# Optimization experiments

Measured on AMD Instinct MI355X. Metric: run time of the kernel, lower is better.

Reference implementation:

```python
import jax, jax.numpy as jnp
import numpy as np

WS = 7
NH = 8
ROPE_FREQ = 100.0


def _rope2d(tokens, positions, freq=ROPE_FREQ):
    # CroCo-style RoPE2D. tokens: [Bw, nh, T, hd]; positions: [Bw, T, 2] int (y, x).
    d = tokens.shape[-1] // 2
    inv = 1.0 / (freq ** (jnp.arange(0, d, 2, dtype=jnp.float32) / d))  # [d/2]

    def rope1d(t, pos):
        ang = pos[..., None].astype(jnp.float32) * inv            # [Bw, T, d/2]
        ang = jnp.concatenate([ang, ang], -1)[:, None]            # [Bw, 1, T, d]
        cos, sin = jnp.cos(ang), jnp.sin(ang)
        x1, x2 = jnp.split(t, 2, axis=-1)
        return t * cos + jnp.concatenate([-x2, x1], -1) * sin

    return jnp.concatenate(
        [rope1d(tokens[..., :d], positions[..., 0]),
         rope1d(tokens[..., d:], positions[..., 1])], -1)


def _qkv(t, w, b, nh):
    Bt, Tt, C = t.shape
    hd = C // nh
    y = (t @ w.T + b).reshape(Bt, Tt, 3, nh, hd).transpose(2, 0, 3, 1, 4)
    return y[0], y[1], y[2]


def _attn(q, k, v, scale):
    a = jax.nn.softmax(jnp.einsum('bhqd,bhkd->bhqk', q, k) * scale, axis=-1)
    return jnp.einsum('bhqk,bhkd->bhqd', a, v)


def setup_inputs() -> dict:
    key = jax.random.key(0)
    ks = jax.random.split(key, 6)
    B, H, W, C, A = 8, 112, 112, 256, 16
    N = H * W + A
    return {
        'x': jax.random.normal(ks[0], (B, N, C), jnp.float32),
        'pos2d': jax.random.randint(ks[1], (B, N, 2), 0, 112, jnp.int32),
        'rope_mask': jnp.ones((B, N), jnp.bool_),
        'qkv_w': jax.random.normal(ks[2], (3 * C, C), jnp.float32) * 0.02,
        'qkv_b': jax.random.normal(ks[3], (3 * C,), jnp.float32) * 0.02,
        'proj_w': jax.random.normal(ks[4], (C, C), jnp.float32) * 0.02,
        'proj_b': jax.random.normal(ks[5], (C,), jnp.float32) * 0.02,
        'grid_h': 112,
        'grid_w': 112,
        'num_added_tokens': 16,
    }


def reference(x, pos2d, rope_mask, qkv_w, qkv_b, proj_w, proj_b, grid_h, grid_w, num_added_tokens):
    B, N, C = x.shape
    H, W, ws, nh = grid_h, grid_w, WS, NH
    hd = C // nh
    scale = hd ** (-0.5)
    HW = H * W
    x_sp, x_add = x[:, :HW], x[:, HW:]
    pos_sp = pos2d[:, :HW]
    mask_sp = rope_mask[:, :HW]

    nWh, nWw = H // ws, W // ws  # H, W divisible by ws (no padding)

    def part(t):  # [B, HW, F] -> [B*nW, ws*ws, F]
        F_ = t.shape[-1]
        t = t.reshape(B, nWh, ws, nWw, ws, F_).transpose(0, 1, 3, 2, 4, 5)
        return t.reshape(B * nWh * nWw, ws * ws, F_)

    xw = part(x_sp)                                   # [Bw, 49, C]
    pw = part(pos_sp)                                 # [Bw, 49, 2]
    mw = part(mask_sp[..., None].astype(jnp.float32))[..., 0] > 0.5  # [Bw, 49]

    q, k, v = _qkv(xw, qkv_w, qkv_b, nh)              # each [Bw, nh, 49, hd]
    qr, kr = _rope2d(q, pw), _rope2d(k, pw)
    m = mw[:, None, :, None]
    q = jnp.where(m, qr, q)
    k = jnp.where(m, kr, k)

    Bw, T = xw.shape[0], ws * ws
    ow = _attn(q, k, v, scale).transpose(0, 2, 1, 3).reshape(Bw, T, C)
    ow = ow @ proj_w.T + proj_b

    # window reverse
    x2 = ow.reshape(B, nWh, nWw, ws, ws, C).transpose(0, 1, 3, 2, 4, 5).reshape(B, HW, C)

    if num_added_tokens > 0:
        qa, ka, va = _qkv(x_add, qkv_w, qkv_b, nh)    # [B, nh, A, hd]
        qs, ks, vs = _qkv(x2, qkv_w, qkv_b, nh)       # [B, nh, HW, hd]
        o_add = _attn(qa, ks, vs, scale).transpose(0, 2, 1, 3).reshape(B, num_added_tokens, C)
        o_add = o_add @ proj_w.T + proj_b
        upd = _attn(qs, ka, va, scale).transpose(0, 2, 1, 3).reshape(B, HW, C)
        upd = upd @ proj_w.T + proj_b
        x2 = x2 + upd * 0.5
        return jnp.concatenate([x2, o_add], axis=1)
    return x2
```

## Files before the change

kernel.cpp:

```cpp
#include <hip/hip_runtime.h>
#include <hip/hip_bf16.h>


typedef __hip_bfloat16 bf16;
typedef __attribute__((ext_vector_type(8))) short short8v;
typedef __attribute__((ext_vector_type(8))) unsigned short ushort8v;
typedef __attribute__((ext_vector_type(4))) float f32x4;

#define HW_TOK 12544
#define NTOK   12560
#define ATT_SCALE 0.17677669529663687f

__device__ __forceinline__ int lwin_to_tok(int wt) {
    int w = wt / 49, t = wt - w * 49;
    int wr = w >> 4, wc = w & 15;
    int r = t / 7, c = t - r * 7;
    return (wr * 7 + r) * 112 + (wc * 7 + c);
}

__device__ __forceinline__ float b2f(unsigned short u) {
    unsigned int w = ((unsigned int)u) << 16;
    return *reinterpret_cast<float*>(&w);
}
__device__ __forceinline__ unsigned short f2b(float v) {
    bf16 h = __float2bfloat16(v);
    return *reinterpret_cast<unsigned short*>(&h);
}

template<bool F32>
__device__ __forceinline__ float ldv(const void* p, size_t i) {
    if constexpr (F32) return reinterpret_cast<const float*>(p)[i];
    else return b2f(reinterpret_cast<const unsigned short*>(p)[i]);
}
template<bool F32>
__device__ __forceinline__ float4 ldv4(const void* p, size_t i) {
    if constexpr (F32) {
        return *reinterpret_cast<const float4*>(reinterpret_cast<const float*>(p) + i);
    } else {
        ushort4 u = *reinterpret_cast<const ushort4*>(
            reinterpret_cast<const unsigned short*>(p) + i);
        return float4{b2f(u.x), b2f(u.y), b2f(u.z), b2f(u.w)};
    }
}
template<bool F32>
__device__ __forceinline__ void stv(void* p, size_t i, float v) {
    if constexpr (F32) reinterpret_cast<float*>(p)[i] = v;
    else reinterpret_cast<unsigned short*>(p)[i] = f2b(v);
}
template<bool F32>
__device__ __forceinline__ void stv4(void* p, size_t i, float4 v) {
    if constexpr (F32) {
        *reinterpret_cast<float4*>(reinterpret_cast<float*>(p) + i) = v;
    } else {
        ushort4 u{f2b(v.x), f2b(v.y), f2b(v.z), f2b(v.w)};
        *reinterpret_cast<ushort4*>(reinterpret_cast<unsigned short*>(p) + i) = u;
    }
}

__global__ void probe_dtype(const unsigned short* x, int n_elem, int* flag) {
    int tid = threadIdx.x;
    int stride = (n_elem / 2048) & ~1;
    if (stride < 2) stride = 2;
    int insane = 0;
    for (int s = 0; s < 8; ++s) {
        long idx = (long)(tid * 8 + s) * stride;
        if (idx >= n_elem) idx = idx % n_elem & ~1L;
        unsigned short u = x[idx];
        unsigned e = (u >> 7) & 0xFF;
        if (e == 0xFF || e >= 141 || (e >= 1 && e <= 112)) insane++;
    }
    __shared__ int tot;
    if (tid == 0) tot = 0;
    __syncthreads();
    atomicAdd(&tot, insane);
    __syncthreads();
    if (tid == 0) flag[0] = (tot > 512) ? 1 : 0;
}

__global__ __launch_bounds__(256) void k_tab(float2* tab) {
    int idx = blockIdx.x * 256 + threadIdx.x;
    if (idx >= 112 * 8) return;
    int p = idx >> 3, i = idx & 7;
    float inv = exp2f((float)i * -0.8304820237218407f);
    float ang = (float)p * inv;
    float sn, cs; sincosf(ang, &sn, &cs);
    tab[idx] = float2{cs, sn};
}

__device__ __forceinline__ f32x4 mfma_bb(short8v a, short8v b, f32x4 c) {
    return __builtin_amdgcn_mfma_f32_16x16x32_bf16(a, b, c, 0, 0, 0);
}
__device__ __forceinline__ f32x4 mfma3(short8v aH, short8v aL,
                                       short8v bH, short8v bL, f32x4 c) {
    c = mfma_bb(aH, bH, c);
    c = mfma_bb(aH, bL, c);
    c = mfma_bb(aL, bH, c);
    return c;
}

__device__ __forceinline__ void cvt8(float4 f0, float4 f1,
                                     ushort8v& hi, ushort8v& lo) {
    float ff[8] = {f0.x, f0.y, f0.z, f0.w, f1.x, f1.y, f1.z, f1.w};
    #pragma unroll
    for (int i = 0; i < 8; ++i) {
        unsigned short h = f2b(ff[i]);
        hi[i] = h;
        lo[i] = f2b(ff[i] - b2f(h));
    }
}

struct __align__(16) GemmLDS {
    unsigned short AsH[128 * 32];
    unsigned short AsL[128 * 32];
    unsigned short BsH[128 * 32];
    unsigned short BsL[128 * 32];
};

__device__ __forceinline__ int lds_idx32(int row, int ks) {
    int byte = (ks * 2) ^ ((row & 3) << 4);
    return row * 32 + (byte >> 1);
}

template<bool F32>
__device__ __forceinline__ void gemm128(
    GemmLDS& L, const void* A, size_t arow, const void* B, size_t brow_,
    f32x4 (&acc)[4][4], int tid)
{
    const int lane = tid & 63, wave = tid >> 6;
    const int wr = (wave >> 1) * 64, wc = (wave & 1) * 64;
    const int fr = lane & 15, fkb = (lane >> 4) * 8;
    const int tr = tid >> 1, tk = (tid & 1) * 16;
    const size_t ab = arow + tk, bb = brow_ + tk;

    float4 pa0, pa1, pa2, pa3, pb0, pb1, pb2, pb3;
    #define LOADCH(K0) do { \
        pa0 = ldv4<F32>(A, ab + (K0));      pa1 = ldv4<F32>(A, ab + (K0) + 4);  \
        pa2 = ldv4<F32>(A, ab + (K0) + 8);  pa3 = ldv4<F32>(A, ab + (K0) + 12); \
        pb0 = ldv4<F32>(B, bb + (K0));      pb1 = ldv4<F32>(B, bb + (K0) + 4);  \
        pb2 = ldv4<F32>(B, bb + (K0) + 8);  pb3 = ldv4<F32>(B, bb + (K0) + 12); \
    } while (0)

    LOADCH(0);
    for (int t = 0; t < 8; ++t) {
        __builtin_amdgcn_s_barrier();
        __builtin_amdgcn_sched_barrier(0);
        ushort8v h, l;
        cvt8(pa0, pa1, h, l);
        *reinterpret_cast<ushort8v*>(&L.AsH[lds_idx32(tr, tk)]) = h;
        *reinterpret_cast<ushort8v*>(&L.AsL[lds_idx32(tr, tk)]) = l;
        cvt8(pa2, pa3, h, l);
        *reinterpret_cast<ushort8v*>(&L.AsH[lds_idx32(tr, tk + 8)]) = h;
        *reinterpret_cast<ushort8v*>(&L.AsL[lds_idx32(tr, tk + 8)]) = l;
        cvt8(pb0, pb1, h, l);
        *reinterpret_cast<ushort8v*>(&L.BsH[lds_idx32(tr, tk)]) = h;
        *reinterpret_cast<ushort8v*>(&L.BsL[lds_idx32(tr, tk)]) = l;
        cvt8(pb2, pb3, h, l);
        *reinterpret_cast<ushort8v*>(&L.BsH[lds_idx32(tr, tk + 8)]) = h;
        *reinterpret_cast<ushort8v*>(&L.BsL[lds_idx32(tr, tk + 8)]) = l;
        if (t < 7) LOADCH((t + 1) * 32);
        asm volatile("s_waitcnt lgkmcnt(0)" ::: "memory");
        __builtin_amdgcn_s_barrier();
        __builtin_amdgcn_sched_barrier(0);
        short8v bH[4], bL[4], aH, aL;
        #pragma unroll
        for (int j = 0; j < 4; ++j) {
            bH[j] = *reinterpret_cast<const short8v*>(&L.BsH[lds_idx32(wc + j * 16 + fr, fkb)]);
            bL[j] = *reinterpret_cast<const short8v*>(&L.BsL[lds_idx32(wc + j * 16 + fr, fkb)]);
        }
        #pragma unroll
        for (int i = 0; i < 4; ++i) {
            aH = *reinterpret_cast<const short8v*>(&L.AsH[lds_idx32(wr + i * 16 + fr, fkb)]);
            aL = *reinterpret_cast<const short8v*>(&L.AsL[lds_idx32(wr + i * 16 + fr, fkb)]);
            #pragma unroll
            for (int j = 0; j < 4; ++j)
                acc[i][j] = mfma3(aH, aL, bH[j], bL[j], acc[i][j]);
        }
    }
    #undef LOADCH
}

__device__ __forceinline__ void epi_coords(int tid, int& rb, int& cb) {
    int lane = tid & 63, wave = tid >> 6;
    rb = (wave >> 1) * 64 + ((lane >> 4) << 2);
    cb = (wave & 1) * 64 + (lane & 15);
}

template<bool F32>
__device__ void k1_body(GemmLDS& L, const void* x, const void* w,
                        const void* bias, void* qkvb, size_t qstride, int b0) {
    int tid = threadIdx.x;
    int n0 = blockIdx.x * 128, m0 = blockIdx.y * 128;
    int z = blockIdx.z, b = b0 + z;
    int tr = tid >> 1;
    size_t arow = (size_t)(b * NTOK + lwin_to_tok(m0 + tr)) * 256;
    size_t brow = (size_t)(n0 + tr) * 256;
    f32x4 acc[4][4] = {};
    gemm128<F32>(L, x, arow, w, brow, acc, tid);
    int rb, cb; epi_coords(tid, rb, cb);
    size_t zb = (size_t)z * qstride;
    #pragma unroll
    for (int j = 0; j < 4; ++j) {
        int n = n0 + cb + j * 16;
        float bi = ldv<F32>(bias, n);
        #pragma unroll
        for (int i = 0; i < 4; ++i)
            #pragma unroll
            for (int r = 0; r < 4; ++r)
                stv<F32>(qkvb, zb + (size_t)(m0 + rb + i * 16 + r) * 768 + n,
                         acc[i][j][r] + bi);
    }
}
__global__ __launch_bounds__(256, 3) void k1_qkv_win(
    const void* x, const void* w, const void* bia, void* qkvb,
    unsigned long long qstride, int b0, const int* flag) {
    __shared__ GemmLDS L;
    if (flag[0]) k1_body<true >(L, x, w, bia, qkvb, qstride, b0);
    else         k1_body<false>(L, x, w, bia, qkvb, qstride, b0);
}

struct K3LDS {
    union {
        struct { unsigned short QH[2048], QL[2048], KH[2048], KL[2048]; } qk;
        struct { unsigned short PH[4096], PL[4096]; } p;
    } u;
    unsigned short VtH[2048], VtL[2048];
};
__device__ __forceinline__ int qk_us(int row, int d) {
    int q16 = (d >> 3) ^ (row & 3);
    return row * 32 + q16 * 8 + (d & 7);
}
__device__ __forceinline__ int p_us(int row, int kk) {
    int q16 = (kk >> 3) ^ (row & 7);
    return row * 64 + q16 * 8 + (kk & 7);
}
__device__ __forceinline__ int vt_us(int d, int kk) {
    int q16 = (kk >> 3) ^ (d & 7);
    return d * 64 + q16 * 8 + (kk & 7);
}

template<bool F32>
__device__ void k3_body(K3LDS& Ld, const void* qkvb, size_t qstride,
                        const int* pos2d, const float2* tab,
                        void* owin, size_t ostride, int b0) {
    int wb = blockIdx.x, h = blockIdx.y, tid = threadIdx.x;
    int z = blockIdx.z, b = b0 + z;
    size_t zq = (size_t)z * qstride, zo = (size_t)z * ostride;
    int lane = tid & 63, w = tid >> 6;
    int l15 = lane & 15, g = lane >> 4;
    int tokbase = ((wb >> 4) * 7) * 112 + (wb & 15) * 7;

    {
        ushort8v z8 = {0, 0, 0, 0, 0, 0, 0, 0};
        ushort8v* vz = reinterpret_cast<ushort8v*>(Ld.VtH);
        for (int e = tid; e < 512; e += 256) vz[e] = z8;
    }
    __syncthreads();

    for (int e0 = tid; e0 < 1280; e0 += 256) {
        int act = (e0 < 1176) ? 1 : 0;
        unsigned ec = act ? (unsigned)e0 : 0u;
        unsigned t = ec / 24u;
        unsigned q = ec - t * 24u;
        int seg = q >> 3, dq = q & 7;
        size_t base = zq + (size_t)(wb * 49 + t) * 768 + seg * 256 + h * 32 + dq * 4;
        float4 f4 = act ? ldv4<F32>(qkvb, base) : float4{0.f, 0.f, 0.f, 0.f};
        if (seg < 2) {
            float4 pf;
            pf.x = __shfl_xor(f4.x, 2); pf.y = __shfl_xor(f4.y, 2);
            pf.z = __shfl_xor(f4.z, 2); pf.w = __shfl_xor(f4.w, 2);
            int half = dq >> 2;
            unsigned r7 = t / 7u, c7 = t - r7 * 7u;
            int ntok = tokbase + (int)r7 * 112 + (int)c7;
            int pos = act ? pos2d[((size_t)b * NTOK + ntok) * 2 + half] : 0;
            const float2* tb = tab + pos * 8 + (dq & 1) * 4;
            float2 s0 = tb[0], s1 = tb[1], s2 = tb[2], s3 = tb[3];
            float sgn = (dq & 2) ? 1.f : -1.f;
            float4 ro;
            ro.x = f4.x * s0.x + sgn * pf.x * s0.y;
            ro.y = f4.y * s1.x + sgn * pf.y * s1.y;
            ro.z = f4.z * s2.x + sgn * pf.z * s2.y;
            ro.w = f4.w * s3.x + sgn * pf.w * s3.y;
            ushort4 hv, lv;
            hv.x = f2b(ro.x); lv.x = f2b(ro.x - b2f(hv.x));
            hv.y = f2b(ro.y); lv.y = f2b(ro.y - b2f(hv.y));
            hv.z = f2b(ro.z); lv.z = f2b(ro.z - b2f(hv.z));
            hv.w = f2b(ro.w); lv.w = f2b(ro.w - b2f(hv.w));
            if (act) {
                unsigned short* H  = seg ? Ld.u.qk.KH : Ld.u.qk.QH;
                unsigned short* Lo = seg ? Ld.u.qk.KL : Ld.u.qk.QL;
                int ua = qk_us(t, dq * 4);
                *reinterpret_cast<ushort4*>(&H[ua])  = hv;
                *reinterpret_cast<ushort4*>(&Lo[ua]) = lv;
            }
        } else if (act) {
            float vv[4] = {f4.x, f4.y, f4.z, f4.w};
            #pragma unroll
            for (int c = 0; c < 4; ++c) {
                int d = dq * 4 + c;
                unsigned short hh = f2b(vv[c]);
                Ld.VtH[vt_us(d, t)] = hh;
                Ld.VtL[vt_us(d, t)] = f2b(vv[c] - b2f(hh));
            }
        }
    }
    __syncthreads();

    f32x4 s[4];
    {
        short8v qH = *reinterpret_cast<const short8v*>(&Ld.u.qk.QH[qk_us(w * 16 + l15, g * 8)]);
        short8v qL = *reinterpret_cast<const short8v*>(&Ld.u.qk.QL[qk_us(w * 16 + l15, g * 8)]);
        #pragma unroll
        for (int j = 0; j < 4; ++j) {
            short8v kH = *reinterpret_cast<const short8v*>(&Ld.u.qk.KH[qk_us(j * 16 + l15, g * 8)]);
            short8v kL = *reinterpret_cast<const short8v*>(&Ld.u.qk.KL[qk_us(j * 16 + l15, g * 8)]);
            f32x4 zz = {0.f, 0.f, 0.f, 0.f};
            s[j] = mfma3(qH, qL, kH, kL, zz);
        }
    }
    #pragma unroll
    for (int j = 0; j < 4; ++j) {
        bool ok = (j * 16 + l15) < 49;
        #pragma unroll
        for (int r = 0; r < 4; ++r)
            s[j][r] = ok ? s[j][r] * ATT_SCALE : -1e30f;
    }
    float rr[4];
    #pragma unroll
    for (int r = 0; r < 4; ++r) {
        float m = fmaxf(fmaxf(s[0][r], s[1][r]), fmaxf(s[2][r], s[3][r]));
        m = fmaxf(m, __shfl_xor(m, 1));
        m = fmaxf(m, __shfl_xor(m, 2));
        m = fmaxf(m, __shfl_xor(m, 4));
        m = fmaxf(m, __shfl_xor(m, 8));
        float sum = 0.f;
        #pragma unroll
        for (int j = 0; j < 4; ++j) {
            float p = __expf(s[j][r] - m);
            s[j][r] = p;
            sum += p;
        }
        sum += __shfl_xor(sum, 1);
        sum += __shfl_xor(sum, 2);
        sum += __shfl_xor(sum, 4);
        sum += __shfl_xor(sum, 8);
        rr[r] = 1.0f / sum;
    }
    __syncthreads();
    #pragma unroll
    for (int j = 0; j < 4; ++j) {
        int col = j * 16 + l15;
        #pragma unroll
        for (int r = 0; r < 4; ++r) {
            int row = w * 16 + 4 * g + r;
            float p = s[j][r] * rr[r];
            unsigned short hh = f2b(p);
            Ld.u.p.PH[p_us(row, col)] = hh;
            Ld.u.p.PL[p_us(row, col)] = f2b(p - b2f(hh));
        }
    }
    __syncthreads();
    f32x4 o[2] = {};
    #pragma unroll
    for (int ks = 0; ks < 2; ++ks) {
        int k0 = ks * 32 + g * 8;
        short8v aH = *reinterpret_cast<const short8v*>(&Ld.u.p.PH[p_us(w * 16 + l15, k0)]);
        short8v aL = *reinterpret_cast<const short8v*>(&Ld.u.p.PL[p_us(w * 16 + l15, k0)]);
        #pragma unroll
        for (int nb = 0; nb < 2; ++nb) {
            short8v bH = *reinterpret_cast<const short8v*>(&Ld.VtH[vt_us(nb * 16 + l15, k0)]);
            short8v bL = *reinterpret_cast<const short8v*>(&Ld.VtL[vt_us(nb * 16 + l15, k0)]);
            o[nb] = mfma3(aH, aL, bH, bL, o[nb]);
        }
    }
    #pragma unroll
    for (int nb = 0; nb < 2; ++nb) {
        int d = nb * 16 + l15;
        #pragma unroll
        for (int r = 0; r < 4; ++r) {
            int row = w * 16 + 4 * g + r;
            if (row < 49)
                stv<F32>(owin, zo + (size_t)(wb * 49 + row) * 256 + h * 32 + d,
                         o[nb][r]);
        }
    }
}
__global__ __launch_bounds__(256, 4) void k3_winattn(
    const void* qkvb, unsigned long long qstride, const int* pos2d,
    const float2* tab, void* owin, unsigned long long ostride, int b0,
    const int* flag) {
    __shared__ K3LDS Ld;
    if (flag[0]) k3_body<true >(Ld, qkvb, qstride, pos2d, tab, owin, ostride, b0);
    else         k3_body<false>(Ld, qkvb, qstride, pos2d, tab, owin, ostride, b0);
}

template<bool F32>
__device__ void k4_body(GemmLDS& L, const void* owin, size_t ostride,
                        const void* w, const void* bias, void* out, int b0) {
    int tid = threadIdx.x;
    int n0 = blockIdx.x * 128, m0 = blockIdx.y * 128;
    int z = blockIdx.z, b = b0 + z;
    int tr = tid >> 1;
    size_t arow = (size_t)z * ostride + (size_t)(m0 + tr) * 256;
    size_t brow = (size_t)(n0 + tr) * 256;
    f32x4 acc[4][4] = {};
    gemm128<F32>(L, owin, arow, w, brow, acc, tid);
    int rb, cb; epi_coords(tid, rb, cb);
    size_t rdst[4][4];
    #pragma unroll
    for (int i = 0; i < 4; ++i)
        #pragma unroll
        for (int r = 0; r < 4; ++r)
            rdst[i][r] = (size_t)(b * NTOK + lwin_to_tok(m0 + rb + i * 16 + r)) * 256;
    #pragma unroll
    for (int j = 0; j < 4; ++j) {
        int n = n0 + cb + j * 16;
        float bi = ldv<F32>(bias, n);
        #pragma unroll
        for (int i = 0; i < 4; ++i)
            #pragma unroll
            for (int r = 0; r < 4; ++r)
                stv<F32>(out, rdst[i][r] + n, acc[i][j][r] + bi);
    }
}
__global__ __launch_bounds__(256, 3) void k4_proj_win(
    const void* owin, unsigned long long ostride, const void* w,
    const void* bia, void* out, int b0, const int* flag) {
    __shared__ GemmLDS L;
    if (flag[0]) k4_body<true >(L, owin, ostride, w, bia, out, b0);
    else         k4_body<false>(L, owin, ostride, w, bia, out, b0);
}

template<bool F32>
__device__ void k5d_body(GemmLDS& L, const void* src, const void* w,
                         const void* bias, void* qkvb, size_t qstride, int b0) {
    int tid = threadIdx.x;
    int n0 = blockIdx.x * 128, m0 = blockIdx.y * 128;
    int z = blockIdx.z, b = b0 + z;
    int tr = tid >> 1;
    size_t arow = ((size_t)b * NTOK + m0 + tr) * 256;
    size_t brow = (size_t)(n0 + tr) * 256;
    f32x4 acc[4][4] = {};
    gemm128<F32>(L, src, arow, w, brow, acc, tid);
    int rb, cb; epi_coords(tid, rb, cb);
    size_t zb = (size_t)z * qstride;
    #pragma unroll
    for (int j = 0; j < 4; ++j) {
        int n = n0 + cb + j * 16;
        float bi = ldv<F32>(bias, n);
        #pragma unroll
        for (int i = 0; i < 4; ++i)
            #pragma unroll
            for (int r = 0; r < 4; ++r)
                stv<F32>(qkvb, zb + (size_t)(m0 + rb + i * 16 + r) * 768 + n,
                         acc[i][j][r] + bi);
    }
}
__global__ __launch_bounds__(256, 3) void k5_dense(
    const void* src, const void* w, const void* bia, void* qkvb,
    unsigned long long qstride, int b0, const int* flag) {
    __shared__ GemmLDS L;
    if (flag[0]) k5d_body<true >(L, src, w, bia, qkvb, qstride, b0);
    else         k5d_body<false>(L, src, w, bia, qkvb, qstride, b0);
}

template<bool F32>
__device__ void k5a_body(GemmLDS& L, const void* x, const void* w,
                         const void* bias, void* dstq, size_t aqbs, int aqroff) {
    int tid = threadIdx.x;
    int n0 = blockIdx.x * 128;
    int tr = tid >> 1;
    int bb = tr >> 4, a = tr & 15;
    size_t arow = ((size_t)bb * NTOK + HW_TOK + a) * 256;
    size_t brow = (size_t)(n0 + tr) * 256;
    f32x4 acc[4][4] = {};
    gemm128<F32>(L, x, arow, w, brow, acc, tid);
    int rb, cb; epi_coords(tid, rb, cb);
    #pragma unroll
    for (int j = 0; j < 4; ++j) {
        int n = n0 + cb + j * 16;
        float bi = ldv<F32>(bias, n);
        #pragma unroll
        for (int i = 0; i < 4; ++i)
            #pragma unroll
            for (int r = 0; r < 4; ++r) {
                int row = rb + i * 16 + r;
                int rbb = row >> 4, ra = row & 15;
                stv<F32>(dstq, (size_t)rbb * aqbs + (size_t)(aqroff + ra) * 768 + n,
                         acc[i][j][r] + bi);
            }
    }
}
__global__ __launch_bounds__(256, 3) void k5_add(
    const void* x, const void* w, const void* bia, void* dstq,
    unsigned long long aqbs, int aqroff, const int* flag) {
    __shared__ GemmLDS L;
    if (flag[0]) k5a_body<true >(L, x, w, bia, dstq, aqbs, aqroff);
    else         k5a_body<false>(L, x, w, bia, dstq, aqbs, aqroff);
}

template<bool F32>
__device__ void k6p_body(const void* addq, size_t aqbs, int aqroff,
                         const void* qkvb, size_t qstride,
                         float* part, size_t pstride, int b0) {
    int h = blockIdx.x, s = blockIdx.y, tid = threadIdx.x;
    int z = blockIdx.z, b = b0 + z;
    size_t zq = (size_t)z * qstride;
    float* pz = part + (size_t)z * pstride;
    __shared__ __align__(16) float qa[16][32];
    __shared__ __align__(16) float ks[49][36];
    __shared__ __align__(16) float vs[49][36];
    __shared__ float S[16][52];
    __shared__ float mrow[16], lrow[16], crow[16];
    int aq = tid >> 3, adg = (tid & 7) * 4;
    if (tid < 128) {
        float4 qv = ldv4<F32>(addq, (size_t)b * aqbs +
                              (size_t)(aqroff + aq) * 768 + h * 32 + adg);
        *reinterpret_cast<float4*>(&qa[aq][adg]) = qv;
    }
    if (tid < 16) { mrow[tid] = -1e30f; lrow[tid] = 0.f; }
    float4 acc{0.f, 0.f, 0.f, 0.f};
    __syncthreads();
    for (int c = 0; c < 4; ++c) {
        int row0 = s * 196 + c * 49;
        for (int e = tid; e < 49 * 8; e += 256) {
            int j = e >> 3, dg = (e & 7) * 4;
            size_t base = zq + (size_t)(row0 + j) * 768 + 256 + h * 32 + dg;
            *reinterpret_cast<float4*>(&ks[j][dg]) = ldv4<F32>(qkvb, base);
            *reinterpret_cast<float4*>(&vs[j][dg]) = ldv4<F32>(qkvb, base + 256);
        }
        __syncthreads();
        for (int e = tid; e < 784; e += 256) {
            int q = e / 49, j = e - q * 49;
            float a = 0.f;
            #pragma unroll
            for (int dg = 0; dg < 8; ++dg) {
                float4 qv = *reinterpret_cast<const float4*>(&qa[q][dg * 4]);
                float4 kv = *reinterpret_cast<const float4*>(&ks[j][dg * 4]);
                a = fmaf(qv.x, kv.x, a); a = fmaf(qv.y, kv.y, a);
                a = fmaf(qv.z, kv.z, a); a = fmaf(qv.w, kv.w, a);
            }
            S[q][j] = a * ATT_SCALE;
        }
        __syncthreads();
        if (tid < 16) {
            float m = mrow[tid], sm = m;
            for (int j = 0; j < 49; ++j) sm = fmaxf(sm, S[tid][j]);
            float corr = expf(m - sm);
            float l = lrow[tid] * corr;
            for (int j = 0; j < 49; ++j) { float p = expf(S[tid][j] - sm); S[tid][j] = p; l += p; }
            mrow[tid] = sm; lrow[tid] = l; crow[tid] = corr;
        }
        __syncthreads();
        if (tid < 128) {
            float cr = crow[aq];
            acc.x *= cr; acc.y *= cr; acc.z *= cr; acc.w *= cr;
            for (int j = 0; j < 49; ++j) {
                float p = S[aq][j];
                float4 v = *reinterpret_cast<const float4*>(&vs[j][adg]);
                acc.x = fmaf(p, v.x, acc.x); acc.y = fmaf(p, v.y, acc.y);
                acc.z = fmaf(p, v.z, acc.z); acc.w = fmaf(p, v.w, acc.w);
            }
        }
        __syncthreads();
    }
    size_t pb = (size_t)(h * 64 + s) * 544;
    if (tid < 128)
        *reinterpret_cast<float4*>(&pz[pb + tid * 4]) = acc;
    if (tid < 16) { pz[pb + 512 + tid] = mrow[tid]; pz[pb + 528 + tid] = lrow[tid]; }
}
__global__ __launch_bounds__(256) void k6_oadd_part(
    const void* addq, unsigned long long aqbs, int aqroff,
    const void* qkvb, unsigned long long qstride,
    float* part, unsigned long long pstride, int b0, const int* flag) {
    if (flag[0]) k6p_body<true >(addq, aqbs, aqroff, qkvb, qstride, part, pstride, b0);
    else         k6p_body<false>(addq, aqbs, aqroff, qkvb, qstride, part, pstride, b0);
}

template<bool F32>
__device__ void k6mb_body(const float* part, size_t pstride,
                          const void* pw, const void* pbias, void* out, int b0) {
    int r = blockIdx.x;
    int zb = r >> 4, a = r & 15;
    int b = b0 + zb;
    const float* P = part + (size_t)zb * pstride;
    int tid = threadIdx.x;
    int h = tid >> 5, d = tid & 31;
    float M = -1e30f;
    for (int s = 0; s < 64; ++s)
        M = fmaxf(M, P[(size_t)(h * 64 + s) * 544 + 512 + a]);
    float o = 0.f, Lsum = 0.f;
    for (int s = 0; s < 64; ++s) {
        size_t pbs = (size_t)(h * 64 + s) * 544;
        float wgt = expf(P[pbs + 512 + a] - M);
        o = fmaf(wgt, P[pbs + a * 32 + d], o);
        Lsum = fmaf(wgt, P[pbs + 528 + a], Lsum);
    }
    __shared__ __align__(16) float orow[256];
    orow[tid] = o / Lsum;
    __syncthreads();
    float acc = ldv<F32>(pbias, tid);
    #pragma unroll 4
    for (int kg = 0; kg < 64; ++kg) {
        float4 w4 = ldv4<F32>(pw, (size_t)tid * 256 + kg * 4);
        float4 o4 = *reinterpret_cast<const float4*>(&orow[kg * 4]);
        acc = fmaf(o4.x, w4.x, acc); acc = fmaf(o4.y, w4.y, acc);
        acc = fmaf(o4.z, w4.z, acc); acc = fmaf(o4.w, w4.w, acc);
    }
    stv<F32>(out, ((size_t)b * NTOK + HW_TOK + a) * 256 + tid, acc);
}
__global__ __launch_bounds__(256) void k6_merge_proj(
    const float* part, unsigned long long pstride, const void* pw,
    const void* pbias, void* out, int b0, const int* flag) {
    if (flag[0]) k6mb_body<true >(part, pstride, pw, pbias, out, b0);
    else         k6mb_body<false>(part, pstride, pw, pbias, out, b0);
}

template<bool F32>
__device__ void k7_body(const void* addq, size_t aqbs, int aqroff,
                        const void* qkvb, size_t qstride,
                        void* updb, size_t ostride, int b0) {
    int tid = threadIdx.x;
    int n0 = blockIdx.x * 32;
    int z = blockIdx.y, b = b0 + z;
    size_t zq = (size_t)z * qstride, zo = (size_t)z * ostride;
    __shared__ __align__(16) float ka[8][16][32];
    __shared__ __align__(16) float va[8][16][32];
    float* kaf = &ka[0][0][0];
    float* vaf = &va[0][0][0];
    for (int e = tid; e < 1024; e += 256) {
        int g = e * 4;
        int h2 = g >> 9, rem = g & 511, a = rem >> 5, d = rem & 31;
        size_t base = (size_t)b * aqbs + (size_t)(aqroff + a) * 768 + 256 + h2 * 32 + d;
        *reinterpret_cast<float4*>(&kaf[g]) = ldv4<F32>(addq, base);
        *reinterpret_cast<float4*>(&vaf[g]) = ldv4<F32>(addq, base + 256);
    }
    __syncthreads();
    int tok = tid & 31, h = tid >> 5;
    int rowl = n0 + tok;
    float q[32];
    #pragma unroll
    for (int dg = 0; dg < 8; ++dg) {
        float4 q4 = ldv4<F32>(qkvb, zq + (size_t)rowl * 768 + h * 32 + dg * 4);
        q[dg * 4 + 0] = q4.x; q[dg * 4 + 1] = q4.y;
        q[dg * 4 + 2] = q4.z; q[dg * 4 + 3] = q4.w;
    }
    float s[16];
    float mx = -1e30f;
    #pragma unroll
    for (int a = 0; a < 16; ++a) {
        float acc = 0.f;
        #pragma unroll
        for (int d = 0; d < 32; ++d) acc = fmaf(q[d], ka[h][a][d], acc);
        s[a] = acc * ATT_SCALE; mx = fmaxf(mx, s[a]);
    }
    float sum = 0.f;
    #pragma unroll
    for (int a = 0; a < 16; ++a) { s[a] = expf(s[a] - mx); sum += s[a]; }
    float r = 1.0f / sum;
    #pragma unroll
    for (int a = 0; a < 16; ++a) s[a] *= r;
    #pragma unroll
    for (int dg = 0; dg < 8; ++dg) {
        float4 o{0.f, 0.f, 0.f, 0.f};
        #pragma unroll
        for (int a = 0; a < 16; ++a) {
            float p = s[a];
            o.x = fmaf(p, va[h][a][dg * 4 + 0], o.x);
            o.y = fmaf(p, va[h][a][dg * 4 + 1], o.y);
            o.z = fmaf(p, va[h][a][dg * 4 + 2], o.z);
            o.w = fmaf(p, va[h][a][dg * 4 + 3], o.w);
        }
        stv4<F32>(updb, zo + (size_t)rowl * 256 + h * 32 + dg * 4, o);
    }
}
__global__ __launch_bounds__(256) void k7_upd(
    const void* addq, unsigned long long aqbs, int aqroff,
    const void* qkvb, unsigned long long qstride,
    void* updb, unsigned long long ostride, int b0, const int* flag) {
    if (flag[0]) k7_body<true >(addq, aqbs, aqroff, qkvb, qstride, updb, ostride, b0);
    else         k7_body<false>(addq, aqbs, aqroff, qkvb, qstride, updb, ostride, b0);
}

template<bool F32>
__device__ void k8_body(GemmLDS& L, const void* updb, size_t ostride,
                        const void* w, const void* bias, void* out, int b0) {
    int tid = threadIdx.x;
    int n0 = blockIdx.x * 128, m0 = blockIdx.y * 128;
    int z = blockIdx.z, b = b0 + z;
    int tr = tid >> 1;
    size_t arow = (size_t)z * ostride + (size_t)(m0 + tr) * 256;
    size_t brow = (size_t)(n0 + tr) * 256;
    f32x4 acc[4][4] = {};
    gemm128<F32>(L, updb, arow, w, brow, acc, tid);
    int rb, cb; epi_coords(tid, rb, cb);
    #pragma unroll
    for (int j = 0; j < 4; ++j) {
        int n = n0 + cb + j * 16;
        float bi = ldv<F32>(bias, n);
        #pragma unroll
        for (int i = 0; i < 4; ++i)
            #pragma unroll
            for (int r = 0; r < 4; ++r) {
                size_t obase = ((size_t)b * NTOK + m0 + rb + i * 16 + r) * 256 + n;
                float xv = ldv<F32>(out, obase);
                stv<F32>(out, obase, xv + 0.5f * (acc[i][j][r] + bi));
            }
    }
}
__global__ __launch_bounds__(256, 3) void k8_final(
    const void* updb, unsigned long long ostride, const void* w,
    const void* bia, void* out, int b0, const int* flag) {
    __shared__ GemmLDS L;
    if (flag[0]) k8_body<true >(L, updb, ostride, w, bia, out, b0);
    else         k8_body<false>(L, updb, ostride, w, bia, out, b0);
}

extern "C" void kernel_launch(void* const* d_in, const int* in_sizes, int n_in,
                              void* d_out, int out_size, void* d_ws, size_t ws_size,
                              hipStream_t stream) {
    const void* x      = d_in[0];
    const int*  pos2d  = (const int*)d_in[1];
    const void* qkv_w  = d_in[3];
    const void* qkv_b  = d_in[4];
    const void* proj_w = d_in[5];
    const void* proj_b = d_in[6];
    void* out = d_out;
    char* wsb = (char*)d_ws;
    (void)n_in; (void)out_size;

    const unsigned long long QS = 12560ull * 768;
    const unsigned long long OS = 12544ull * 256;
    const unsigned long long PS = 8ull * 64 * 544;

    const size_t MERGED_NEED = 411442240ull;

    if (ws_size >= MERGED_NEED) {
        void*   qkvb = (void*)wsb;
        void*   owin = (void*)(wsb + 308674560);
        void*   updb = owin;
        float*  part = (float*)owin;
        int*    flag = (int*)(wsb + 308674560 + 102760448);
        float2* tab  = (float2*)(wsb + 411435072);

        probe_dtype<<<dim3(1), 256, 0, stream>>>((const unsigned short*)x,
                                                 in_sizes[0], flag);
        k_tab<<<dim3(4), 256, 0, stream>>>(tab);
        k5_add<<<dim3(6, 1), 256, 0, stream>>>(x, qkv_w, qkv_b, qkvb,
                                               QS, HW_TOK, flag);
        k1_qkv_win<<<dim3(6, 98, 8), 256, 0, stream>>>(
            x, qkv_w, qkv_b, qkvb, QS, 0, flag);
        k3_winattn<<<dim3(256, 8, 8), 256, 0, stream>>>(
            qkvb, QS, pos2d, tab, owin, OS, 0, flag);
        k4_proj_win<<<dim3(2, 98, 8), 256, 0, stream>>>(
            owin, OS, proj_w, proj_b, out, 0, flag);
        k5_dense<<<dim3(6, 98, 8), 256, 0, stream>>>(
            out, qkv_w, qkv_b, qkvb, QS, 0, flag);
        k6_oadd_part<<<dim3(8, 64, 8), 256, 0, stream>>>(
            qkvb, QS, HW_TOK, qkvb, QS, part, PS, 0, flag);
        k6_merge_proj<<<dim3(128), 256, 0, stream>>>(
            part, PS, proj_w, proj_b, out, 0, flag);
        k7_upd<<<dim3(392, 8), 256, 0, stream>>>(
            qkvb, QS, HW_TOK, qkvb, QS, updb, OS, 0, flag);
        k8_final<<<dim3(2, 98, 8), 256, 0, stream>>>(
            updb, OS, proj_w, proj_b, out, 0, flag);
    } else {
        void*   qkvb = (void*)wsb;
        void*   owin = (void*)(wsb + 38535168);
        void*   updb = owin;
        float*  part = (float*)owin;
        void*   qadd = (void*)(wsb + 51380224);
        float2* tab  = (float2*)(wsb + 51773440);
        int*    flag = (int*)(wsb + 52183040);
        const unsigned long long AQB = 16ull * 768;

        probe_dtype<<<dim3(1), 256, 0, stream>>>((const unsigned short*)x,
                                                 in_sizes[0], flag);
        k_tab<<<dim3(4), 256, 0, stream>>>(tab);
        k5_add<<<dim3(6, 1), 256, 0, stream>>>(x, qkv_w, qkv_b, qadd,
                                               AQB, 0, flag);
        for (int b = 0; b < 8; ++b) {
            k1_qkv_win<<<dim3(6, 98, 1), 256, 0, stream>>>(
                x, qkv_w, qkv_b, qkvb, 0, b, flag);
            k3_winattn<<<dim3(256, 8, 1), 256, 0, stream>>>(
                qkvb, 0, pos2d, tab, owin, 0, b, flag);
            k4_proj_win<<<dim3(2, 98, 1), 256, 0, stream>>>(
                owin, 0, proj_w, proj_b, out, b, flag);
            k5_dense<<<dim3(6, 98, 1), 256, 0, stream>>>(
                out, qkv_w, qkv_b, qkvb, 0, b, flag);
            k6_oadd_part<<<dim3(8, 64, 1), 256, 0, stream>>>(
                qadd, AQB, 0, qkvb, 0, part, 0, b, flag);
            k6_merge_proj<<<dim3(16), 256, 0, stream>>>(
                part, 0, proj_w, proj_b, out, b, flag);
            k7_upd<<<dim3(392, 1), 256, 0, stream>>>(
                qadd, AQB, 0, qkvb, 0, updb, 0, b, flag);
            k8_final<<<dim3(2, 98, 1), 256, 0, stream>>>(
                updb, 0, proj_w, proj_b, out, b, flag);
        }
    }
}
```

Measured before the change: 1.042 ms.

## Swizzle GEMM LDS layout, remap block order, parallelize softmax, use fast exp

Changes the GEMM shared-memory index swizzle to a two-rows-per-64-element layout with an XOR over 8 banks groups, to reduce LDS bank conflicts. Flattens the GEMM grids into 1D with batch as the fastest-varying index so that concurrently resident blocks share weight tiles, aiming at better L2 reuse. Spreads the online softmax in the added-token attention across 8 threads per row with shuffle reductions instead of 16 serial threads. Replaces expf with __expf in several places, which trades a little accuracy for cheaper exponentials.

```diff
diff --git a/kernel.cpp b/kernel.cpp
--- a/kernel.cpp
+++ b/kernel.cpp
@@ -117,8 +117,9 @@
 };
 
 __device__ __forceinline__ int lds_idx32(int row, int ks) {
-    int byte = (ks * 2) ^ ((row & 3) << 4);
-    return row * 32 + (byte >> 1);
+    int lb = ((row & 1) << 6) | (ks << 1);
+    lb ^= ((row >> 1) & 7) << 4;
+    return ((row >> 1) << 6) + (lb >> 1);
 }
 
 template<bool F32>
@@ -185,12 +186,34 @@
     cb = (wave & 1) * 64 + (lane & 15);
 }
 
+__device__ __forceinline__ void k1_coords(int swz, int& n0, int& m0, int& z) {
+    if (swz) {
+        z = blockIdx.x & 7;
+        int r = blockIdx.x >> 3;
+        n0 = (r % 6) * 128;
+        m0 = (r / 6) * 128;
+    } else {
+        n0 = blockIdx.x * 128; m0 = blockIdx.y * 128; z = blockIdx.z;
+    }
+}
+__device__ __forceinline__ void k4_coords(int swz, int& n0, int& m0, int& z) {
+    if (swz) {
+        z = blockIdx.x & 7;
+        int r = blockIdx.x >> 3;
+        n0 = (r & 1) * 128;
+        m0 = (r >> 1) * 128;
+    } else {
+        n0 = blockIdx.x * 128; m0 = blockIdx.y * 128; z = blockIdx.z;
+    }
+}
+
 template<bool F32>
 __device__ void k1_body(GemmLDS& L, const void* x, const void* w,
-                        const void* bias, void* qkvb, size_t qstride, int b0) {
+                        const void* bias, void* qkvb, size_t qstride, int b0,
+                        int swz) {
     int tid = threadIdx.x;
-    int n0 = blockIdx.x * 128, m0 = blockIdx.y * 128;
-    int z = blockIdx.z, b = b0 + z;
+    int n0, m0, z; k1_coords(swz, n0, m0, z);
+    int b = b0 + z;
     int tr = tid >> 1;
     size_t arow = (size_t)(b * NTOK + lwin_to_tok(m0 + tr)) * 256;
     size_t brow = (size_t)(n0 + tr) * 256;
@@ -212,10 +235,10 @@
 }
 __global__ __launch_bounds__(256, 3) void k1_qkv_win(
     const void* x, const void* w, const void* bia, void* qkvb,
-    unsigned long long qstride, int b0, const int* flag) {
+    unsigned long long qstride, int b0, int swz, const int* flag) {
     __shared__ GemmLDS L;
-    if (flag[0]) k1_body<true >(L, x, w, bia, qkvb, qstride, b0);
-    else         k1_body<false>(L, x, w, bia, qkvb, qstride, b0);
+    if (flag[0]) k1_body<true >(L, x, w, bia, qkvb, qstride, b0, swz);
+    else         k1_body<false>(L, x, w, bia, qkvb, qstride, b0, swz);
 }
 
 struct K3LDS {
@@ -395,10 +418,11 @@
 
 template<bool F32>
 __device__ void k4_body(GemmLDS& L, const void* owin, size_t ostride,
-                        const void* w, const void* bias, void* out, int b0) {
+                        const void* w, const void* bias, void* out, int b0,
+                        int swz) {
     int tid = threadIdx.x;
-    int n0 = blockIdx.x * 128, m0 = blockIdx.y * 128;
-    int z = blockIdx.z, b = b0 + z;
+    int n0, m0, z; k4_coords(swz, n0, m0, z);
+    int b = b0 + z;
     int tr = tid >> 1;
     size_t arow = (size_t)z * ostride + (size_t)(m0 + tr) * 256;
     size_t brow = (size_t)(n0 + tr) * 256;
@@ -424,18 +448,19 @@
 }
 __global__ __launch_bounds__(256, 3) void k4_proj_win(
     const void* owin, unsigned long long ostride, const void* w,
-    const void* bia, void* out, int b0, const int* flag) {
+    const void* bia, void* out, int b0, int swz, const int* flag) {
     __shared__ GemmLDS L;
-    if (flag[0]) k4_body<true >(L, owin, ostride, w, bia, out, b0);
-    else         k4_body<false>(L, owin, ostride, w, bia, out, b0);
+    if (flag[0]) k4_body<true >(L, owin, ostride, w, bia, out, b0, swz);
+    else         k4_body<false>(L, owin, ostride, w, bia, out, b0, swz);
 }
 
 template<bool F32>
 __device__ void k5d_body(GemmLDS& L, const void* src, const void* w,
-                         const void* bias, void* qkvb, size_t qstride, int b0) {
+                         const void* bias, void* qkvb, size_t qstride, int b0,
+                         int swz) {
     int tid = threadIdx.x;
-    int n0 = blockIdx.x * 128, m0 = blockIdx.y * 128;
-    int z = blockIdx.z, b = b0 + z;
+    int n0, m0, z; k1_coords(swz, n0, m0, z);
+    int b = b0 + z;
     int tr = tid >> 1;
     size_t arow = ((size_t)b * NTOK + m0 + tr) * 256;
     size_t brow = (size_t)(n0 + tr) * 256;
@@ -457,10 +482,10 @@
 }
 __global__ __launch_bounds__(256, 3) void k5_dense(
     const void* src, const void* w, const void* bia, void* qkvb,
-    unsigned long long qstride, int b0, const int* flag) {
+    unsigned long long qstride, int b0, int swz, const int* flag) {
     __shared__ GemmLDS L;
-    if (flag[0]) k5d_body<true >(L, src, w, bia, qkvb, qstride, b0);
-    else         k5d_body<false>(L, src, w, bia, qkvb, qstride, b0);
+    if (flag[0]) k5d_body<true >(L, src, w, bia, qkvb, qstride, b0, swz);
+    else         k5d_body<false>(L, src, w, bia, qkvb, qstride, b0, swz);
 }
 
 template<bool F32>
@@ -542,13 +567,29 @@
             S[q][j] = a * ATT_SCALE;
         }
         __syncthreads();
-        if (tid < 16) {
-            float m = mrow[tid], sm = m;
-            for (int j = 0; j < 49; ++j) sm = fmaxf(sm, S[tid][j]);
-            float corr = expf(m - sm);
-            float l = lrow[tid] * corr;
-            for (int j = 0; j < 49; ++j) { float p = expf(S[tid][j] - sm); S[tid][j] = p; l += p; }
-            mrow[tid] = sm; lrow[tid] = l; crow[tid] = corr;
+        if (tid < 128) {
+            int row = tid >> 3, sub = tid & 7;
+            float lm = -1e30f;
+            for (int j = sub; j < 49; j += 8) lm = fmaxf(lm, S[row][j]);
+            lm = fmaxf(lm, __shfl_xor(lm, 1));
+            lm = fmaxf(lm, __shfl_xor(lm, 2));
+            lm = fmaxf(lm, __shfl_xor(lm, 4));
+            float sm = fmaxf(mrow[row], lm);
+            float ls = 0.f;
+            for (int j = sub; j < 49; j += 8) {
+                float p = __expf(S[row][j] - sm);
+                S[row][j] = p;
+                ls += p;
+            }
+            ls += __shfl_xor(ls, 1);
+            ls += __shfl_xor(ls, 2);
+            ls += __shfl_xor(ls, 4);
+            if (sub == 0) {
+                float corr = __expf(mrow[row] - sm);
+                crow[row] = corr;
+                lrow[row] = lrow[row] * corr + ls;
+                mrow[row] = sm;
+            }
         }
         __syncthreads();
         if (tid < 128) {
@@ -591,7 +632,7 @@
     float o = 0.f, Lsum = 0.f;
     for (int s = 0; s < 64; ++s) {
         size_t pbs = (size_t)(h * 64 + s) * 544;
-        float wgt = expf(P[pbs + 512 + a] - M);
+        float wgt = __expf(P[pbs + 512 + a] - M);
         o = fmaf(wgt, P[pbs + a * 32 + d], o);
         Lsum = fmaf(wgt, P[pbs + 528 + a], Lsum);
     }
@@ -655,7 +696,7 @@
     }
     float sum = 0.f;
     #pragma unroll
-    for (int a = 0; a < 16; ++a) { s[a] = expf(s[a] - mx); sum += s[a]; }
+    for (int a = 0; a < 16; ++a) { s[a] = __expf(s[a] - mx); sum += s[a]; }
     float r = 1.0f / sum;
     #pragma unroll
     for (int a = 0; a < 16; ++a) s[a] *= r;
@@ -683,10 +724,11 @@
 
 template<bool F32>
 __device__ void k8_body(GemmLDS& L, const void* updb, size_t ostride,
-                        const void* w, const void* bias, void* out, int b0) {
+                        const void* w, const void* bias, void* out, int b0,
+                        int swz) {
     int tid = threadIdx.x;
-    int n0 = blockIdx.x * 128, m0 = blockIdx.y * 128;
-    int z = blockIdx.z, b = b0 + z;
+    int n0, m0, z; k4_coords(swz, n0, m0, z);
+    int b = b0 + z;
     int tr = tid >> 1;
     size_t arow = (size_t)z * ostride + (size_t)(m0 + tr) * 256;
     size_t brow = (size_t)(n0 + tr) * 256;
@@ -709,10 +751,10 @@
 }
 __global__ __launch_bounds__(256, 3) void k8_final(
     const void* updb, unsigned long long ostride, const void* w,
-    const void* bia, void* out, int b0, const int* flag) {
+    const void* bia, void* out, int b0, int swz, const int* flag) {
     __shared__ GemmLDS L;
-    if (flag[0]) k8_body<true >(L, updb, ostride, w, bia, out, b0);
-    else         k8_body<false>(L, updb, ostride, w, bia, out, b0);
+    if (flag[0]) k8_body<true >(L, updb, ostride, w, bia, out, b0, swz);
+    else         k8_body<false>(L, updb, ostride, w, bia, out, b0, swz);
 }
 
 extern "C" void kernel_launch(void* const* d_in, const int* in_sizes, int n_in,
@@ -747,22 +789,22 @@
         k_tab<<<dim3(4), 256, 0, stream>>>(tab);
         k5_add<<<dim3(6, 1), 256, 0, stream>>>(x, qkv_w, qkv_b, qkvb,
                                                QS, HW_TOK, flag);
-        k1_qkv_win<<<dim3(6, 98, 8), 256, 0, stream>>>(
-            x, qkv_w, qkv_b, qkvb, QS, 0, flag);
+        k1_qkv_win<<<dim3(4704), 256, 0, stream>>>(
+            x, qkv_w, qkv_b, qkvb, QS, 0, 1, flag);
         k3_winattn<<<dim3(256, 8, 8), 256, 0, stream>>>(
             qkvb, QS, pos2d, tab, owin, OS, 0, flag);
-        k4_proj_win<<<dim3(2, 98, 8), 256, 0, stream>>>(
-            owin, OS, proj_w, proj_b, out, 0, flag);
-        k5_dense<<<dim3(6, 98, 8), 256, 0, stream>>>(
-            out, qkv_w, qkv_b, qkvb, QS, 0, flag);
+        k4_proj_win<<<dim3(1568), 256, 0, stream>>>(
+            owin, OS, proj_w, proj_b, out, 0, 1, flag);
+        k5_dense<<<dim3(4704), 256, 0, stream>>>(
+            out, qkv_w, qkv_b, qkvb, QS, 0, 1, flag);
         k6_oadd_part<<<dim3(8, 64, 8), 256, 0, stream>>>(
             qkvb, QS, HW_TOK, qkvb, QS, part, PS, 0, flag);
         k6_merge_proj<<<dim3(128), 256, 0, stream>>>(
             part, PS, proj_w, proj_b, out, 0, flag);
         k7_upd<<<dim3(392, 8), 256, 0, stream>>>(
             qkvb, QS, HW_TOK, qkvb, QS, updb, OS, 0, flag);
-        k8_final<<<dim3(2, 98, 8), 256, 0, stream>>>(
-            updb, OS, proj_w, proj_b, out, 0, flag);
+        k8_final<<<dim3(1568), 256, 0, stream>>>(
+            updb, OS, proj_w, proj_b, out, 0, 1, flag);
     } else {
         void*   qkvb = (void*)wsb;
         void*   owin = (void*)(wsb + 38535168);
@@ -780,13 +822,13 @@
                                                AQB, 0, flag);
         for (int b = 0; b < 8; ++b) {
             k1_qkv_win<<<dim3(6, 98, 1), 256, 0, stream>>>(
-                x, qkv_w, qkv_b, qkvb, 0, b, flag);
+                x, qkv_w, qkv_b, qkvb, 0, b, 0, flag);
             k3_winattn<<<dim3(256, 8, 1), 256, 0, stream>>>(
                 qkvb, 0, pos2d, tab, owin, 0, b, flag);
             k4_proj_win<<<dim3(2, 98, 1), 256, 0, stream>>>(
-                owin, 0, proj_w, proj_b, out, b, flag);
+                owin, 0, proj_w, proj_b, out, b, 0, flag);
             k5_dense<<<dim3(6, 98, 1), 256, 0, stream>>>(
-                out, qkv_w, qkv_b, qkvb, 0, b, flag);
+                out, qkv_w, qkv_b, qkvb, 0, b, 0, flag);
             k6_oadd_part<<<dim3(8, 64, 1), 256, 0, stream>>>(
                 qadd, AQB, 0, qkvb, 0, part, 0, b, flag);
             k6_merge_proj<<<dim3(16), 256, 0, stream>>>(
@@ -794,7 +836,7 @@
             k7_upd<<<dim3(392, 1), 256, 0, stream>>>(
                 qadd, AQB, 0, qkvb, 0, updb, 0, b, flag);
             k8_final<<<dim3(2, 98, 1), 256, 0, stream>>>(
-                updb, 0, proj_w, proj_b, out, b, flag);
-        }
-    }
-}
+                updb, 0, proj_w, proj_b, out, b, 0, flag);
+        }
+    }
+}
```

New measurement: 998.7 us. 1.04x faster.
